# Kernel tuning notes

Measured on AMD Instinct MI355X. Metric: run time of the kernel, lower is better.

The kernel has to match this reference:

```python
import jax, jax.numpy as jnp
from jax import lax
import numpy as np
import math

D_MODEL = 1024
D_STATE = 16
DT_RANK = 64  # ceil(1024/16)


def setup_inputs() -> dict:
    key = jax.random.key(0)
    ks = jax.random.split(key, 8)
    B, L = 2, 2048
    x = jax.random.normal(ks[0], (B, L, D_MODEL), dtype=jnp.float32)
    A_log = jnp.full((D_MODEL, D_STATE), math.log(0.5), dtype=jnp.float32)
    x_proj_w = jax.random.normal(ks[1], (DT_RANK + 2 * D_STATE, D_MODEL), dtype=jnp.float32) * (D_MODEL ** -0.5)
    dt_init_std = DT_RANK ** -0.5
    dt_proj_w = jax.random.uniform(ks[2], (D_MODEL, DT_RANK), minval=-dt_init_std, maxval=dt_init_std, dtype=jnp.float32)
    # dt bias init: softplus-inverse of dt sampled log-uniform in [2*dt_min, 2*dt_max] (trend)
    dt = jnp.exp(jax.random.uniform(ks[3], (D_MODEL,), dtype=jnp.float32) * (math.log(0.2) - math.log(0.002)) + math.log(0.002))
    dt = jnp.clip(dt, 1e-4)
    dt_proj_b = dt + jnp.log(-jnp.expm1(-dt))
    D_param = jnp.ones((D_MODEL,), dtype=jnp.float32)
    trend_emphasis = jnp.full((D_MODEL,), 0.1, dtype=jnp.float32)
    return {
        "x": x, "A_log": A_log, "x_proj_w": x_proj_w,
        "dt_proj_w": dt_proj_w, "dt_proj_b": dt_proj_b,
        "D_param": D_param, "trend_emphasis": trend_emphasis,
    }


def _selective_scan(u, delta, A, Bp, Cp, D_param):
    # u, delta: [B,L,D]; A: [D,N]; Bp, Cp: [B,L,N]; D_param: [D]
    deltaA = jnp.exp(jnp.einsum('bld,dn->bldn', delta, A))       # [B,L,D,N]
    deltaBu = jnp.einsum('bld,bln->bldn', delta * u, Bp)          # [B,L,D,N]
    Bsz, L, Dm, N = deltaA.shape

    def step(h, inp):
        dA, dBu, c = inp          # dA,dBu: [B,D,N]; c: [B,N]
        h = dA * h + dBu
        y = jnp.einsum('bdn,bn->bd', h, c)
        return h, y

    h0 = jnp.zeros((Bsz, Dm, N), dtype=u.dtype)
    xs = (jnp.moveaxis(deltaA, 1, 0), jnp.moveaxis(deltaBu, 1, 0), jnp.moveaxis(Cp, 1, 0))
    _, ys = lax.scan(step, h0, xs)            # ys: [L,B,D]
    y = jnp.moveaxis(ys, 0, 1)                # [B,L,D]
    return y + u * D_param


def reference(x, A_log, x_proj_w, dt_proj_w, dt_proj_b, D_param, trend_emphasis):
    # trend component: channel-wise emphasis gate (dropout in eval mode = identity)
    x = x * jax.nn.sigmoid(trend_emphasis)
    xz = x @ x_proj_w.T                                  # [B,L,dt_rank+2N]
    delta_part = xz[..., :DT_RANK]
    Bp = xz[..., DT_RANK:DT_RANK + D_STATE]              # [B,L,N]
    Cp = xz[..., DT_RANK + D_STATE:]                     # [B,L,N]
    delta = jax.nn.softplus(delta_part @ dt_proj_w.T + dt_proj_b)  # [B,L,D]
    A = -jnp.exp(A_log.astype(jnp.float32))
    return _selective_scan(x, delta, A, Bp, Cp, D_param.astype(jnp.float32))
```

## Files before the change

kernel.cpp:

```cpp
#include <hip/hip_runtime.h>
#include <math.h>


#define LOG2E 1.44269504088896340736f
typedef float v2f __attribute__((ext_vector_type(2)));

__device__ __forceinline__ float fexp2(float v){
#if defined(__has_builtin)
#if __has_builtin(__builtin_amdgcn_exp2f)
  return __builtin_amdgcn_exp2f(v);
#else
  return exp2f(v);
#endif
#else
  return exp2f(v);
#endif
}

__device__ __forceinline__ float fsoftplus(float v){
  return fmaxf(v, 0.f) + __logf(1.f + __expf(-fabsf(v)));
}

__global__ __launch_bounds__(256) void k_prep(const float* __restrict__ xpw,
                                              const float* __restrict__ dtw,
                                              const float* __restrict__ alog,
                                              const float* __restrict__ te,
                                              float* __restrict__ w2T,
                                              float* __restrict__ dtwT,
                                              float* __restrict__ A2,
                                              float* __restrict__ sg){
  __shared__ float sm[32 * 33];
  const int bid = blockIdx.x, t = threadIdx.x;
  const int lane = t & 31, srow = t >> 5;
  if (bid < 96){
    const int kt = bid / 3, ct = bid - kt * 3;
#pragma unroll
    for (int r = 0; r < 4; r++){
      const int cr = srow * 4 + r;
      sm[cr * 33 + lane] = xpw[(size_t)(ct * 32 + cr) * 1024 + kt * 32 + lane];
    }
    __syncthreads();
#pragma unroll
    for (int r = 0; r < 4; r++){
      const int kr = srow * 4 + r;
      const int kg = kt * 32 + kr;
      const float s = 1.f / (1.f + __expf(-te[kg]));
      w2T[(size_t)kg * 96 + ct * 32 + lane] = sm[lane * 33 + kr] * s;
    }
  } else if (bid < 160){
    const int idx = bid - 96, dti = idx >> 1, kt2 = idx & 1;
#pragma unroll
    for (int r = 0; r < 4; r++){
      const int cr = srow * 4 + r;
      sm[cr * 33 + lane] = dtw[(size_t)(dti * 32 + cr) * 64 + kt2 * 32 + lane];
    }
    __syncthreads();
#pragma unroll
    for (int r = 0; r < 4; r++){
      const int kr = srow * 4 + r;
      dtwT[(size_t)(kt2 * 32 + kr) * 1024 + dti * 32 + lane] = sm[lane * 33 + kr];
    }
  } else if (bid < 176){
    const int j = (bid - 160) * 1024 + t;
#pragma unroll
    for (int i = 0; i < 4; i++)
      A2[j + i * 256] = -__expf(alog[j + i * 256]) * LOG2E;
  } else {
#pragma unroll
    for (int i = 0; i < 4; i++){
      const int m = i * 256 + t;
      sg[m] = 1.f / (1.f + __expf(-te[m]));
    }
  }
}

__global__ __launch_bounds__(256) void k_xz(const float* __restrict__ x,
                                            const float* __restrict__ w2T,
                                            float* __restrict__ xzp){
  __shared__ float xT[32 * 257];
  const int t = threadIdx.x;
  const int row0 = blockIdx.x * 256;
  const int c0 = blockIdx.y * 32;
  const int kbase = blockIdx.z * 128;
  v2f acc[16];
#pragma unroll
  for (int c = 0; c < 16; c++) acc[c] = (v2f){0.f, 0.f};
  const int kq = t & 7, rsub = t >> 3;
  for (int kt = 0; kt < 4; ++kt){
    const int k0 = kbase + kt * 32;
    __syncthreads();
#pragma unroll
    for (int p = 0; p < 8; p++){
      const int r = p * 32 + rsub;
      const float4 v = *reinterpret_cast<const float4*>(&x[(size_t)(row0 + r) * 1024 + k0 + kq * 4]);
      xT[(kq * 4 + 0) * 257 + r] = v.x;
      xT[(kq * 4 + 1) * 257 + r] = v.y;
      xT[(kq * 4 + 2) * 257 + r] = v.z;
      xT[(kq * 4 + 3) * 257 + r] = v.w;
    }
    __syncthreads();
#pragma unroll 4
    for (int kk = 0; kk < 32; ++kk){
      const float xv = xT[kk * 257 + t];
      const v2f xv2 = {xv, xv};
      const v2f* wr = reinterpret_cast<const v2f*>(&w2T[(size_t)(k0 + kk) * 96 + c0]);
#pragma unroll
      for (int c = 0; c < 16; c++) acc[c] = acc[c] + xv2 * wr[c];
    }
  }
  float4* o = reinterpret_cast<float4*>(xzp + ((size_t)blockIdx.z * 4096 + row0 + t) * 96 + c0);
  const float4* av = reinterpret_cast<const float4*>(acc);
#pragma unroll
  for (int q = 0; q < 8; q++) o[q] = av[q];
}

__global__ __launch_bounds__(256) void k_reduce(const float4* __restrict__ p,
                                                float4* __restrict__ xz){
  const int i = blockIdx.x * 256 + threadIdx.x;
  float4 r = p[i];
#pragma unroll
  for (int s = 1; s < 8; s++){
    const float4 a = p[(size_t)s * 98304 + i];
    r.x += a.x; r.y += a.y; r.z += a.z; r.w += a.w;
  }
  xz[i] = r;
}

__global__ __launch_bounds__(256) void k_delta(const float* __restrict__ xz,
                                               const float* __restrict__ dtwT,
                                               const float* __restrict__ dtb,
                                               float* __restrict__ del){
  const int t = threadIdx.x;
  const int r0 = blockIdx.x * 16;
  const int d = blockIdx.y * 256 + t;
  v2f wv[32];
#pragma unroll
  for (int k2 = 0; k2 < 32; k2++){
    wv[k2].x = dtwT[(size_t)(2 * k2) * 1024 + d];
    wv[k2].y = dtwT[(size_t)(2 * k2 + 1) * 1024 + d];
  }
  const float dtbv = dtb[d];
  const float* xzb = xz + (size_t)r0 * 96;
#pragma unroll 4
  for (int li = 0; li < 16; ++li){
    v2f acc = {dtbv, 0.f};
    const v2f* dp = reinterpret_cast<const v2f*>(xzb + li * 96);
#pragma unroll
    for (int k2 = 0; k2 < 32; k2++) acc = acc + dp[k2] * wv[k2];
    del[(size_t)(r0 + li) * 1024 + d] = fsoftplus(acc.x + acc.y);
  }
}

__global__ __launch_bounds__(256) void k_scan1(const float* __restrict__ x,
                                               const float* __restrict__ del,
                                               const float* __restrict__ xz,
                                               const float* __restrict__ A2,
                                               const float* __restrict__ sg,
                                               float* __restrict__ S,
                                               float* __restrict__ P){
  __shared__ float bsm[32 * 16];
  const int t = threadIdx.x;
  const int chunk = blockIdx.x, dgrp = blockIdx.y, b = blockIdx.z;
  const int d = dgrp * 256 + t;
  const int l0 = chunk * 32;
  const float* xzb = xz + (size_t)(b * 2048 + l0) * 96;

  if (t < 128){
    const int r = t >> 2, c4 = t & 3;
    *reinterpret_cast<float4*>(&bsm[r * 16 + c4 * 4]) =
      *reinterpret_cast<const float4*>(xzb + r * 96 + 64 + c4 * 4);
  }

  float a2[16];
  {
    const float4* ap = reinterpret_cast<const float4*>(A2 + (size_t)d * 16);
#pragma unroll
    for (int q = 0; q < 4; q++){
      const float4 v = ap[q];
      a2[q*4] = v.x; a2[q*4+1] = v.y; a2[q*4+2] = v.z; a2[q*4+3] = v.w;
    }
  }
  bool uni = true;
#pragma unroll
  for (int n = 1; n < 16; n++) uni = uni && (a2[n] == a2[0]);
  const float sgv = sg[d];
  const size_t xidx0 = (size_t)(b * 2048 + l0) * 1024 + d;
  const size_t base = ((size_t)((b * 64 + chunk) * 1024 + d)) * 16;

  __syncthreads();

  if (uni){
    const float a2u = a2[0];
    v2f h2[8];
#pragma unroll
    for (int q = 0; q < 8; q++) h2[q] = (v2f){0.f, 0.f};
    float sumd = 0.f;
    for (int ph = 0; ph < 2; ++ph){
      const size_t xidx = xidx0 + (size_t)ph * 16 * 1024;
      float dl[16], du[16];
#pragma unroll
      for (int li = 0; li < 16; ++li){
        dl[li] = del[xidx + (size_t)li * 1024];
        du[li] = dl[li] * x[xidx + (size_t)li * 1024] * sgv;
      }
#pragma unroll 4
      for (int li = 0; li < 16; ++li){
        sumd += dl[li];
        const float tt = fexp2(dl[li] * a2u);
        const v2f tt2 = {tt, tt}, du2 = {du[li], du[li]};
        const v2f* brow = reinterpret_cast<const v2f*>(&bsm[(ph * 16 + li) * 16]);
#pragma unroll
        for (int q = 0; q < 8; q++) h2[q] = h2[q] * tt2 + brow[q] * du2;
      }
    }
    const float4* hv = reinterpret_cast<const float4*>(h2);
#pragma unroll
    for (int q = 0; q < 4; q++)
      *reinterpret_cast<float4*>(&S[base + q * 4]) = hv[q];
    const float Ppu = fexp2(a2u * sumd);
    const float4 pv = {Ppu, Ppu, Ppu, Ppu};
#pragma unroll
    for (int q = 0; q < 4; q++)
      *reinterpret_cast<float4*>(&P[base + q * 4]) = pv;
  } else {
    float h[16], Pp[16];
#pragma unroll
    for (int n = 0; n < 16; n++){ h[n] = 0.f; Pp[n] = 1.f; }
    for (int li = 0; li < 32; ++li){
      const float dv = del[xidx0 + (size_t)li * 1024];
      const float duv = dv * x[xidx0 + (size_t)li * 1024] * sgv;
      const float* brow = &bsm[li * 16];
#pragma unroll
      for (int n = 0; n < 16; n++){
        const float tt = fexp2(dv * a2[n]);
        h[n] = fmaf(tt, h[n], duv * brow[n]);
        Pp[n] *= tt;
      }
    }
#pragma unroll
    for (int q = 0; q < 4; q++){
      float4 v; v.x = h[q*4]; v.y = h[q*4+1]; v.z = h[q*4+2]; v.w = h[q*4+3];
      *reinterpret_cast<float4*>(&S[base + q * 4]) = v;
      float4 u; u.x = Pp[q*4]; u.y = Pp[q*4+1]; u.z = Pp[q*4+2]; u.w = Pp[q*4+3];
      *reinterpret_cast<float4*>(&P[base + q * 4]) = u;
    }
  }
}

__global__ __launch_bounds__(256) void k_scan2(const float* __restrict__ S,
                                               const float* __restrict__ P,
                                               float* __restrict__ H){
  __shared__ float ls[256], lp[256];
  const int t = threadIdx.x;
  const int dn = t & 31, seg = t >> 5;
  const int n = dn & 15, dloc = dn >> 4;
  const int bid = blockIdx.x;
  const int b = bid >> 9, dpair = bid & 511;
  const int d = dpair * 2 + dloc;
  const size_t sbase = ((size_t)(b * 64) * 1024 + d) * 16 + n;
  float Sv[8], Pv[8];
  float s = 0.f, p = 1.f;
#pragma unroll
  for (int i = 0; i < 8; i++){
    const size_t idx = sbase + (size_t)(seg * 8 + i) * 16384;
    Sv[i] = S[idx]; Pv[i] = P[idx];
    s = fmaf(Pv[i], s, Sv[i]);
    p *= Pv[i];
  }
  ls[t] = s; lp[t] = p;
  __syncthreads();
  float h = 0.f;
  for (int j = 0; j < seg; j++)
    h = fmaf(lp[j * 32 + dn], h, ls[j * 32 + dn]);
#pragma unroll
  for (int i = 0; i < 8; i++){
    const size_t idx = sbase + (size_t)(seg * 8 + i) * 16384;
    H[idx] = h;
    h = fmaf(Pv[i], h, Sv[i]);
  }
}

__global__ __launch_bounds__(256) void k_scan3(const float* __restrict__ x,
                                               const float* __restrict__ del,
                                               const float* __restrict__ xz,
                                               const float* __restrict__ A2,
                                               const float* __restrict__ sg,
                                               const float* __restrict__ Dpar,
                                               const float* __restrict__ H,
                                               float* __restrict__ out){
  __shared__ float bcs[32 * 32];
  const int t = threadIdx.x;
  const int chunk = blockIdx.x, dgrp = blockIdx.y, b = blockIdx.z;
  const int d = dgrp * 256 + t;
  const int l0 = chunk * 32;
  const float* xzb = xz + (size_t)(b * 2048 + l0) * 96;

  {
    const int r = t >> 3, c4 = t & 7;
    *reinterpret_cast<float4*>(&bcs[r * 32 + c4 * 4]) =
      *reinterpret_cast<const float4*>(xzb + r * 96 + 64 + c4 * 4);
  }

  float a2[16];
  {
    const float4* ap = reinterpret_cast<const float4*>(A2 + (size_t)d * 16);
#pragma unroll
    for (int q = 0; q < 4; q++){
      const float4 v = ap[q];
      a2[q*4] = v.x; a2[q*4+1] = v.y; a2[q*4+2] = v.z; a2[q*4+3] = v.w;
    }
  }
  bool uni = true;
#pragma unroll
  for (int n = 1; n < 16; n++) uni = uni && (a2[n] == a2[0]);
  const float sgv = sg[d], Dv = Dpar[d];
  const size_t xidx0 = (size_t)(b * 2048 + l0) * 1024 + d;
  const size_t hbase = ((size_t)((b * 64 + chunk) * 1024 + d)) * 16;

  __syncthreads();

  if (uni){
    const float a2u = a2[0];
    v2f h2[8];
    {
      const float4* hp = reinterpret_cast<const float4*>(H + hbase);
      float4* hd = reinterpret_cast<float4*>(h2);
#pragma unroll
      for (int q = 0; q < 4; q++) hd[q] = hp[q];
    }
    for (int ph = 0; ph < 2; ++ph){
      const size_t xidx = xidx0 + (size_t)ph * 16 * 1024;
      float dl[16], xd[16];
#pragma unroll
      for (int li = 0; li < 16; ++li){
        dl[li] = del[xidx + (size_t)li * 1024];
        xd[li] = x[xidx + (size_t)li * 1024] * sgv;
      }
#pragma unroll 4
      for (int li = 0; li < 16; ++li){
        const float duv = dl[li] * xd[li];
        const float tt = fexp2(dl[li] * a2u);
        const v2f tt2 = {tt, tt}, du2 = {duv, duv};
        const v2f* brow = reinterpret_cast<const v2f*>(&bcs[(ph * 16 + li) * 32]);
        const v2f* crow = reinterpret_cast<const v2f*>(&bcs[(ph * 16 + li) * 32 + 16]);
        v2f yv = {0.f, 0.f};
#pragma unroll
        for (int q = 0; q < 8; q++){
          h2[q] = h2[q] * tt2 + brow[q] * du2;
          yv = yv + h2[q] * crow[q];
        }
        out[xidx + (size_t)li * 1024] = fmaf(xd[li], Dv, yv.x + yv.y);
      }
    }
  } else {
    float h[16];
    {
      const float4* hp = reinterpret_cast<const float4*>(H + hbase);
#pragma unroll
      for (int q = 0; q < 4; q++){
        const float4 v = hp[q];
        h[q*4] = v.x; h[q*4+1] = v.y; h[q*4+2] = v.z; h[q*4+3] = v.w;
      }
    }
    for (int li = 0; li < 32; ++li){
      const float dv = del[xidx0 + (size_t)li * 1024];
      const float xdv = x[xidx0 + (size_t)li * 1024] * sgv;
      const float duv = dv * xdv;
      const float* brow = &bcs[li * 32];
      float y = 0.f;
#pragma unroll
      for (int n = 0; n < 16; n++){
        const float tt = fexp2(dv * a2[n]);
        h[n] = fmaf(tt, h[n], duv * brow[n]);
        y = fmaf(h[n], brow[16 + n], y);
      }
      out[xidx0 + (size_t)li * 1024] = fmaf(xdv, Dv, y);
    }
  }
}

extern "C" void kernel_launch(void* const* d_in, const int* in_sizes, int n_in,
                              void* d_out, int out_size, void* d_ws, size_t ws_size,
                              hipStream_t stream){
  const float* x    = (const float*)d_in[0];
  const float* Alog = (const float*)d_in[1];
  const float* xpw  = (const float*)d_in[2];
  const float* dtw  = (const float*)d_in[3];
  const float* dtb  = (const float*)d_in[4];
  const float* Dpar = (const float*)d_in[5];
  const float* te   = (const float*)d_in[6];
  float* out = (float*)d_out;
  char* ws = (char*)d_ws;

  float* w2T  = (float*)(ws);
  float* A2   = (float*)(ws + 393216);
  float* sg   = (float*)(ws + 458752);
  float* dtwT = (float*)(ws + 462848);
  float* xz   = (float*)(ws + 724992);
  float* del  = (float*)(ws + 2297856);
  float* xzp  = (float*)(ws + 19075072);
  float* S    = (float*)(ws + 31657984);
  float* P    = (float*)(ws + 40046592);
  float* Hst  = (float*)(ws + 48435200);

  hipLaunchKernelGGL(k_prep,   dim3(177),        dim3(256), 0, stream, xpw, dtw, Alog, te, w2T, dtwT, A2, sg);
  hipLaunchKernelGGL(k_xz,     dim3(16, 3, 8),   dim3(256), 0, stream, x, w2T, xzp);
  hipLaunchKernelGGL(k_reduce, dim3(384),        dim3(256), 0, stream, (const float4*)xzp, (float4*)xz);
  hipLaunchKernelGGL(k_delta,  dim3(256, 4),     dim3(256), 0, stream, xz, dtwT, dtb, del);
  hipLaunchKernelGGL(k_scan1,  dim3(64, 4, 2),   dim3(256), 0, stream, x, del, xz, A2, sg, S, P);
  hipLaunchKernelGGL(k_scan2,  dim3(1024),       dim3(256), 0, stream, S, P, Hst);
  hipLaunchKernelGGL(k_scan3,  dim3(64, 4, 2),   dim3(256), 0, stream, x, del, xz, A2, sg, Dpar, Hst, out);
}
```

Before: 152.5 us.

## Store delta in per-chunk channel-major layout and stage xz rows in LDS

The delta kernel now stages its 16 rows of the dt-rank projection in shared memory. It writes delta in a blocked layout of [16-row block][channel][16], so each thread emits four float4 stores. Both scan kernels read delta with matching float4 loads instead of sixteen strided scalar loads. This trades coalesced per-row access for wide per-thread vector accesses, which may give uncoalesced stride-64B patterns across lanes.

```diff
diff --git a/kernel.cpp b/kernel.cpp
--- a/kernel.cpp
+++ b/kernel.cpp
@@ -130,9 +130,17 @@
                                                const float* __restrict__ dtwT,
                                                const float* __restrict__ dtb,
                                                float* __restrict__ del){
+  __shared__ float xd[16 * 64];
   const int t = threadIdx.x;
   const int r0 = blockIdx.x * 16;
   const int d = blockIdx.y * 256 + t;
+
+  {
+    const int r = t >> 4, c4 = t & 15;
+    *reinterpret_cast<float4*>(&xd[r * 64 + c4 * 4]) =
+      *reinterpret_cast<const float4*>(xz + (size_t)(r0 + r) * 96 + c4 * 4);
+  }
+
   v2f wv[32];
 #pragma unroll
   for (int k2 = 0; k2 < 32; k2++){
@@ -140,15 +148,23 @@
     wv[k2].y = dtwT[(size_t)(2 * k2 + 1) * 1024 + d];
   }
   const float dtbv = dtb[d];
-  const float* xzb = xz + (size_t)r0 * 96;
+
+  __syncthreads();
+
+  float dl[16];
 #pragma unroll 4
   for (int li = 0; li < 16; ++li){
     v2f acc = {dtbv, 0.f};
-    const v2f* dp = reinterpret_cast<const v2f*>(xzb + li * 96);
+    const v2f* dp = reinterpret_cast<const v2f*>(&xd[li * 64]);
 #pragma unroll
     for (int k2 = 0; k2 < 32; k2++) acc = acc + dp[k2] * wv[k2];
-    del[(size_t)(r0 + li) * 1024 + d] = fsoftplus(acc.x + acc.y);
-  }
+    dl[li] = fsoftplus(acc.x + acc.y);
+  }
+
+  float4* o = reinterpret_cast<float4*>(del + (size_t)blockIdx.x * 16384 + (size_t)d * 16);
+  const float4* dv4 = reinterpret_cast<const float4*>(dl);
+#pragma unroll
+  for (int q = 0; q < 4; q++) o[q] = dv4[q];
 }
 
 __global__ __launch_bounds__(256) void k_scan1(const float* __restrict__ x,
@@ -163,6 +179,7 @@
   const int chunk = blockIdx.x, dgrp = blockIdx.y, b = blockIdx.z;
   const int d = dgrp * 256 + t;
   const int l0 = chunk * 32;
+  const int j0 = b * 128 + chunk * 2;
   const float* xzb = xz + (size_t)(b * 2048 + l0) * 96;
 
   if (t < 128){
@@ -198,11 +215,15 @@
     for (int ph = 0; ph < 2; ++ph){
       const size_t xidx = xidx0 + (size_t)ph * 16 * 1024;
       float dl[16], du[16];
-#pragma unroll
-      for (int li = 0; li < 16; ++li){
-        dl[li] = del[xidx + (size_t)li * 1024];
+      {
+        const float4* dp = reinterpret_cast<const float4*>(del + (size_t)(j0 + ph) * 16384 + (size_t)d * 16);
+        float4* o = reinterpret_cast<float4*>(dl);
+#pragma unroll
+        for (int q = 0; q < 4; q++) o[q] = dp[q];
+      }
+#pragma unroll
+      for (int li = 0; li < 16; ++li)
         du[li] = dl[li] * x[xidx + (size_t)li * 1024] * sgv;
-      }
 #pragma unroll 4
       for (int li = 0; li < 16; ++li){
         sumd += dl[li];
@@ -226,8 +247,16 @@
     float h[16], Pp[16];
 #pragma unroll
     for (int n = 0; n < 16; n++){ h[n] = 0.f; Pp[n] = 1.f; }
+    float dla[32];
+#pragma unroll
+    for (int hh = 0; hh < 2; hh++){
+      const float4* dp = reinterpret_cast<const float4*>(del + (size_t)(j0 + hh) * 16384 + (size_t)d * 16);
+      float4* o = reinterpret_cast<float4*>(dla + hh * 16);
+#pragma unroll
+      for (int q = 0; q < 4; q++) o[q] = dp[q];
+    }
     for (int li = 0; li < 32; ++li){
-      const float dv = del[xidx0 + (size_t)li * 1024];
+      const float dv = dla[li];
       const float duv = dv * x[xidx0 + (size_t)li * 1024] * sgv;
       const float* brow = &bsm[li * 16];
 #pragma unroll
@@ -293,6 +322,7 @@
   const int chunk = blockIdx.x, dgrp = blockIdx.y, b = blockIdx.z;
   const int d = dgrp * 256 + t;
   const int l0 = chunk * 32;
+  const int j0 = b * 128 + chunk * 2;
   const float* xzb = xz + (size_t)(b * 2048 + l0) * 96;
 
   {
@@ -331,11 +361,15 @@
     for (int ph = 0; ph < 2; ++ph){
       const size_t xidx = xidx0 + (size_t)ph * 16 * 1024;
       float dl[16], xd[16];
-#pragma unroll
-      for (int li = 0; li < 16; ++li){
-        dl[li] = del[xidx + (size_t)li * 1024];
+      {
+        const float4* dp = reinterpret_cast<const float4*>(del + (size_t)(j0 + ph) * 16384 + (size_t)d * 16);
+        float4* o = reinterpret_cast<float4*>(dl);
+#pragma unroll
+        for (int q = 0; q < 4; q++) o[q] = dp[q];
+      }
+#pragma unroll
+      for (int li = 0; li < 16; ++li)
         xd[li] = x[xidx + (size_t)li * 1024] * sgv;
-      }
 #pragma unroll 4
       for (int li = 0; li < 16; ++li){
         const float duv = dl[li] * xd[li];
@@ -362,8 +396,16 @@
         h[q*4] = v.x; h[q*4+1] = v.y; h[q*4+2] = v.z; h[q*4+3] = v.w;
       }
     }
+    float dla[32];
+#pragma unroll
+    for (int hh = 0; hh < 2; hh++){
+      const float4* dp = reinterpret_cast<const float4*>(del + (size_t)(j0 + hh) * 16384 + (size_t)d * 16);
+      float4* o = reinterpret_cast<float4*>(dla + hh * 16);
+#pragma unroll
+      for (int q = 0; q < 4; q++) o[q] = dp[q];
+    }
     for (int li = 0; li < 32; ++li){
-      const float dv = del[xidx0 + (size_t)li * 1024];
+      const float dv = dla[li];
       const float xdv = x[xidx0 + (size_t)li * 1024] * sgv;
       const float duv = dv * xdv;
       const float* brow = &bcs[li * 32];
```

Measured after the change: 225.8 us. 1.48x slower.

## Split state dimension across threads in chunked scan kernels

Applied to the files above, without the earlier changes.

The chunk scan kernels now assign several threads to each channel. scan1 uses 4 threads with 4 states each, and scan3 uses 2 threads with 8 states each, combining outputs with a lane shuffle. The grids grow to match, and launch bounds request higher occupancy. The goal is more parallelism and fewer registers per thread in the latency-bound scan phases. The cost is redundant loads of delta and x per thread, plus the shuffle and half-idle stores in scan3.

```diff
diff --git a/kernel.cpp b/kernel.cpp
--- a/kernel.cpp
+++ b/kernel.cpp
@@ -151,17 +151,18 @@
   }
 }
 
-__global__ __launch_bounds__(256) void k_scan1(const float* __restrict__ x,
-                                               const float* __restrict__ del,
-                                               const float* __restrict__ xz,
-                                               const float* __restrict__ A2,
-                                               const float* __restrict__ sg,
-                                               float* __restrict__ S,
-                                               float* __restrict__ P){
+__global__ __launch_bounds__(256, 4) void k_scan1(const float* __restrict__ x,
+                                                  const float* __restrict__ del,
+                                                  const float* __restrict__ xz,
+                                                  const float* __restrict__ A2,
+                                                  const float* __restrict__ sg,
+                                                  float* __restrict__ S,
+                                                  float* __restrict__ P){
   __shared__ float bsm[32 * 16];
   const int t = threadIdx.x;
   const int chunk = blockIdx.x, dgrp = blockIdx.y, b = blockIdx.z;
-  const int d = dgrp * 256 + t;
+  const int ng = t & 3;
+  const int d = dgrp * 64 + (t >> 2);
   const int l0 = chunk * 32;
   const float* xzb = xz + (size_t)(b * 2048 + l0) * 96;
 
@@ -171,79 +172,63 @@
       *reinterpret_cast<const float4*>(xzb + r * 96 + 64 + c4 * 4);
   }
 
-  float a2[16];
+  float a2[4];
   {
-    const float4* ap = reinterpret_cast<const float4*>(A2 + (size_t)d * 16);
-#pragma unroll
-    for (int q = 0; q < 4; q++){
-      const float4 v = ap[q];
-      a2[q*4] = v.x; a2[q*4+1] = v.y; a2[q*4+2] = v.z; a2[q*4+3] = v.w;
-    }
-  }
-  bool uni = true;
-#pragma unroll
-  for (int n = 1; n < 16; n++) uni = uni && (a2[n] == a2[0]);
+    const float4 v = *reinterpret_cast<const float4*>(A2 + (size_t)d * 16 + ng * 4);
+    a2[0] = v.x; a2[1] = v.y; a2[2] = v.z; a2[3] = v.w;
+  }
+  const bool uni = (a2[1] == a2[0]) && (a2[2] == a2[0]) && (a2[3] == a2[0]);
   const float sgv = sg[d];
   const size_t xidx0 = (size_t)(b * 2048 + l0) * 1024 + d;
-  const size_t base = ((size_t)((b * 64 + chunk) * 1024 + d)) * 16;
+  const size_t base = ((size_t)((b * 64 + chunk) * 1024 + d)) * 16 + ng * 4;
 
   __syncthreads();
 
   if (uni){
     const float a2u = a2[0];
-    v2f h2[8];
-#pragma unroll
-    for (int q = 0; q < 8; q++) h2[q] = (v2f){0.f, 0.f};
+    v2f h2[2];
+    h2[0] = (v2f){0.f, 0.f}; h2[1] = (v2f){0.f, 0.f};
     float sumd = 0.f;
-    for (int ph = 0; ph < 2; ++ph){
-      const size_t xidx = xidx0 + (size_t)ph * 16 * 1024;
-      float dl[16], du[16];
-#pragma unroll
-      for (int li = 0; li < 16; ++li){
+    for (int ph = 0; ph < 4; ++ph){
+      const size_t xidx = xidx0 + (size_t)ph * 8 * 1024;
+      float dl[8], du[8];
+#pragma unroll
+      for (int li = 0; li < 8; ++li){
         dl[li] = del[xidx + (size_t)li * 1024];
         du[li] = dl[li] * x[xidx + (size_t)li * 1024] * sgv;
       }
-#pragma unroll 4
-      for (int li = 0; li < 16; ++li){
+#pragma unroll
+      for (int li = 0; li < 8; ++li){
         sumd += dl[li];
         const float tt = fexp2(dl[li] * a2u);
         const v2f tt2 = {tt, tt}, du2 = {du[li], du[li]};
-        const v2f* brow = reinterpret_cast<const v2f*>(&bsm[(ph * 16 + li) * 16]);
-#pragma unroll
-        for (int q = 0; q < 8; q++) h2[q] = h2[q] * tt2 + brow[q] * du2;
-      }
-    }
-    const float4* hv = reinterpret_cast<const float4*>(h2);
-#pragma unroll
-    for (int q = 0; q < 4; q++)
-      *reinterpret_cast<float4*>(&S[base + q * 4]) = hv[q];
+        const v2f* brow = reinterpret_cast<const v2f*>(&bsm[(ph * 8 + li) * 16 + ng * 4]);
+        h2[0] = h2[0] * tt2 + brow[0] * du2;
+        h2[1] = h2[1] * tt2 + brow[1] * du2;
+      }
+    }
+    *reinterpret_cast<float4*>(&S[base]) = *reinterpret_cast<const float4*>(h2);
     const float Ppu = fexp2(a2u * sumd);
-    const float4 pv = {Ppu, Ppu, Ppu, Ppu};
-#pragma unroll
-    for (int q = 0; q < 4; q++)
-      *reinterpret_cast<float4*>(&P[base + q * 4]) = pv;
+    *reinterpret_cast<float4*>(&P[base]) = (float4){Ppu, Ppu, Ppu, Ppu};
   } else {
-    float h[16], Pp[16];
-#pragma unroll
-    for (int n = 0; n < 16; n++){ h[n] = 0.f; Pp[n] = 1.f; }
+    float h[4], Pp[4];
+#pragma unroll
+    for (int n = 0; n < 4; n++){ h[n] = 0.f; Pp[n] = 1.f; }
     for (int li = 0; li < 32; ++li){
       const float dv = del[xidx0 + (size_t)li * 1024];
       const float duv = dv * x[xidx0 + (size_t)li * 1024] * sgv;
-      const float* brow = &bsm[li * 16];
-#pragma unroll
-      for (int n = 0; n < 16; n++){
+      const float* brow = &bsm[li * 16 + ng * 4];
+#pragma unroll
+      for (int n = 0; n < 4; n++){
         const float tt = fexp2(dv * a2[n]);
         h[n] = fmaf(tt, h[n], duv * brow[n]);
         Pp[n] *= tt;
       }
     }
-#pragma unroll
-    for (int q = 0; q < 4; q++){
-      float4 v; v.x = h[q*4]; v.y = h[q*4+1]; v.z = h[q*4+2]; v.w = h[q*4+3];
-      *reinterpret_cast<float4*>(&S[base + q * 4]) = v;
-      float4 u; u.x = Pp[q*4]; u.y = Pp[q*4+1]; u.z = Pp[q*4+2]; u.w = Pp[q*4+3];
-      *reinterpret_cast<float4*>(&P[base + q * 4]) = u;
-    }
+    float4 v; v.x = h[0]; v.y = h[1]; v.z = h[2]; v.w = h[3];
+    *reinterpret_cast<float4*>(&S[base]) = v;
+    float4 u; u.x = Pp[0]; u.y = Pp[1]; u.z = Pp[2]; u.w = Pp[3];
+    *reinterpret_cast<float4*>(&P[base]) = u;
   }
 }
 
@@ -280,18 +265,19 @@
   }
 }
 
-__global__ __launch_bounds__(256) void k_scan3(const float* __restrict__ x,
-                                               const float* __restrict__ del,
-                                               const float* __restrict__ xz,
-                                               const float* __restrict__ A2,
-                                               const float* __restrict__ sg,
-                                               const float* __restrict__ Dpar,
-                                               const float* __restrict__ H,
-                                               float* __restrict__ out){
+__global__ __launch_bounds__(256, 4) void k_scan3(const float* __restrict__ x,
+                                                  const float* __restrict__ del,
+                                                  const float* __restrict__ xz,
+                                                  const float* __restrict__ A2,
+                                                  const float* __restrict__ sg,
+                                                  const float* __restrict__ Dpar,
+                                                  const float* __restrict__ H,
+                                                  float* __restrict__ out){
   __shared__ float bcs[32 * 32];
   const int t = threadIdx.x;
   const int chunk = blockIdx.x, dgrp = blockIdx.y, b = blockIdx.z;
-  const int d = dgrp * 256 + t;
+  const int ng = t & 1;
+  const int d = dgrp * 128 + (t >> 1);
   const int l0 = chunk * 32;
   const float* xzb = xz + (size_t)(b * 2048 + l0) * 96;
 
@@ -301,63 +287,65 @@
       *reinterpret_cast<const float4*>(xzb + r * 96 + 64 + c4 * 4);
   }
 
-  float a2[16];
+  float a2[8];
   {
-    const float4* ap = reinterpret_cast<const float4*>(A2 + (size_t)d * 16);
-#pragma unroll
-    for (int q = 0; q < 4; q++){
+    const float4* ap = reinterpret_cast<const float4*>(A2 + (size_t)d * 16 + ng * 8);
+#pragma unroll
+    for (int q = 0; q < 2; q++){
       const float4 v = ap[q];
       a2[q*4] = v.x; a2[q*4+1] = v.y; a2[q*4+2] = v.z; a2[q*4+3] = v.w;
     }
   }
   bool uni = true;
 #pragma unroll
-  for (int n = 1; n < 16; n++) uni = uni && (a2[n] == a2[0]);
+  for (int n = 1; n < 8; n++) uni = uni && (a2[n] == a2[0]);
   const float sgv = sg[d], Dv = Dpar[d];
   const size_t xidx0 = (size_t)(b * 2048 + l0) * 1024 + d;
-  const size_t hbase = ((size_t)((b * 64 + chunk) * 1024 + d)) * 16;
+  const size_t hbase = ((size_t)((b * 64 + chunk) * 1024 + d)) * 16 + ng * 8;
 
   __syncthreads();
 
   if (uni){
     const float a2u = a2[0];
-    v2f h2[8];
+    v2f h2[4];
     {
       const float4* hp = reinterpret_cast<const float4*>(H + hbase);
       float4* hd = reinterpret_cast<float4*>(h2);
-#pragma unroll
-      for (int q = 0; q < 4; q++) hd[q] = hp[q];
-    }
-    for (int ph = 0; ph < 2; ++ph){
-      const size_t xidx = xidx0 + (size_t)ph * 16 * 1024;
-      float dl[16], xd[16];
-#pragma unroll
-      for (int li = 0; li < 16; ++li){
+      hd[0] = hp[0]; hd[1] = hp[1];
+    }
+    for (int ph = 0; ph < 4; ++ph){
+      const size_t xidx = xidx0 + (size_t)ph * 8 * 1024;
+      float dl[8], xd[8];
+#pragma unroll
+      for (int li = 0; li < 8; ++li){
         dl[li] = del[xidx + (size_t)li * 1024];
         xd[li] = x[xidx + (size_t)li * 1024] * sgv;
       }
-#pragma unroll 4
-      for (int li = 0; li < 16; ++li){
+#pragma unroll
+      for (int li = 0; li < 8; ++li){
         const float duv = dl[li] * xd[li];
         const float tt = fexp2(dl[li] * a2u);
         const v2f tt2 = {tt, tt}, du2 = {duv, duv};
-        const v2f* brow = reinterpret_cast<const v2f*>(&bcs[(ph * 16 + li) * 32]);
-        const v2f* crow = reinterpret_cast<const v2f*>(&bcs[(ph * 16 + li) * 32 + 16]);
+        const v2f* brow = reinterpret_cast<const v2f*>(&bcs[(ph * 8 + li) * 32 + ng * 8]);
+        const v2f* crow = reinterpret_cast<const v2f*>(&bcs[(ph * 8 + li) * 32 + 16 + ng * 8]);
         v2f yv = {0.f, 0.f};
 #pragma unroll
-        for (int q = 0; q < 8; q++){
+        for (int q = 0; q < 4; q++){
           h2[q] = h2[q] * tt2 + brow[q] * du2;
           yv = yv + h2[q] * crow[q];
         }
-        out[xidx + (size_t)li * 1024] = fmaf(xd[li], Dv, yv.x + yv.y);
+        float y = yv.x + yv.y;
+        y += __shfl_xor(y, 1);
+        if (ng == 0)
+          out[xidx + (size_t)li * 1024] = fmaf(xd[li], Dv, y);
       }
     }
   } else {
-    float h[16];
+    float h[8];
     {
       const float4* hp = reinterpret_cast<const float4*>(H + hbase);
 #pragma unroll
-      for (int q = 0; q < 4; q++){
+      for (int q = 0; q < 2; q++){
         const float4 v = hp[q];
         h[q*4] = v.x; h[q*4+1] = v.y; h[q*4+2] = v.z; h[q*4+3] = v.w;
       }
@@ -366,15 +354,17 @@
       const float dv = del[xidx0 + (size_t)li * 1024];
       const float xdv = x[xidx0 + (size_t)li * 1024] * sgv;
       const float duv = dv * xdv;
-      const float* brow = &bcs[li * 32];
+      const float* brow = &bcs[li * 32 + ng * 8];
       float y = 0.f;
 #pragma unroll
-      for (int n = 0; n < 16; n++){
+      for (int n = 0; n < 8; n++){
         const float tt = fexp2(dv * a2[n]);
         h[n] = fmaf(tt, h[n], duv * brow[n]);
         y = fmaf(h[n], brow[16 + n], y);
       }
-      out[xidx0 + (size_t)li * 1024] = fmaf(xdv, Dv, y);
+      y += __shfl_xor(y, 1);
+      if (ng == 0)
+        out[xidx0 + (size_t)li * 1024] = fmaf(xdv, Dv, y);
     }
   }
 }
@@ -407,7 +397,7 @@
   hipLaunchKernelGGL(k_xz,     dim3(16, 3, 8),   dim3(256), 0, stream, x, w2T, xzp);
   hipLaunchKernelGGL(k_reduce, dim3(384),        dim3(256), 0, stream, (const float4*)xzp, (float4*)xz);
   hipLaunchKernelGGL(k_delta,  dim3(256, 4),     dim3(256), 0, stream, xz, dtwT, dtb, del);
-  hipLaunchKernelGGL(k_scan1,  dim3(64, 4, 2),   dim3(256), 0, stream, x, del, xz, A2, sg, S, P);
+  hipLaunchKernelGGL(k_scan1,  dim3(64, 16, 2),  dim3(256), 0, stream, x, del, xz, A2, sg, S, P);
   hipLaunchKernelGGL(k_scan2,  dim3(1024),       dim3(256), 0, stream, S, P, Hst);
-  hipLaunchKernelGGL(k_scan3,  dim3(64, 4, 2),   dim3(256), 0, stream, x, del, xz, A2, sg, Dpar, Hst, out);
-}
+  hipLaunchKernelGGL(k_scan3,  dim3(64, 8, 2),   dim3(256), 0, stream, x, del, xz, A2, sg, Dpar, Hst, out);
+}
```

New measurement: 150.7 us, median of 2. About the same (-1.1%).
